# Optimization experiments

Measured on AMD Instinct MI355X. Metric: run time of the kernel, lower is better.

## Reference

```python
import jax, jax.numpy as jnp
import numpy as np

N = 50000   # nodes
E = 800000  # edges (before self loops)
IN_DIM = 64
HID = 128
HEADS = 4
DH = HID // HEADS  # 32 per-head out_feats
L = 3
EPS = 1e-5
NEG_SLOPE = 0.2


def setup_inputs() -> dict:
    key = jax.random.key(0)
    ks = jax.random.split(key, 10)
    s = 0.1  # weight scale for numerical sanity
    return {
        "node_feats": jax.random.normal(ks[0], (N, IN_DIM), jnp.float32),
        "src": jax.random.randint(ks[1], (E,), 0, N, dtype=jnp.int32),
        "dst": jax.random.randint(ks[2], (E,), 0, N, dtype=jnp.int32),
        "W_in": jax.random.normal(ks[3], (IN_DIM, HID), jnp.float32) * s,
        "b_in": jnp.zeros((HID,), jnp.float32),
        "W_src": jax.random.normal(ks[4], (L, HID, HID), jnp.float32) * s,
        "b_src": jnp.zeros((L, HID), jnp.float32),
        "W_dst": jax.random.normal(ks[5], (L, HID, HID), jnp.float32) * s,
        "b_dst": jnp.zeros((L, HID), jnp.float32),
        "attn": jax.random.normal(ks[6], (L, HEADS, DH), jnp.float32) * s,
        "ln_g": jnp.ones((L, HID), jnp.float32),
        "ln_b": jnp.zeros((L, HID), jnp.float32),
    }


def _layer_norm(x, g, b):
    mu = jnp.mean(x, axis=-1, keepdims=True)
    var = jnp.mean((x - mu) ** 2, axis=-1, keepdims=True)
    return (x - mu) * jax.lax.rsqrt(var + EPS) * g + b


def _gatv2(h, s_idx, d_idx, Ws, bs, Wd, bd, a):
    # h: [N, HID]; edges s_idx -> d_idx (self loops included)
    fs = (h @ Ws + bs).reshape(N, HEADS, DH)  # W_src h, source features
    fd = (h @ Wd + bd).reshape(N, HEADS, DH)  # W_dst h, dest features
    e = jax.nn.leaky_relu(fs[s_idx] + fd[d_idx], NEG_SLOPE)   # [E', H, D]
    logits = jnp.einsum('ehd,hd->eh', e, a)                   # [E', H]
    # segment softmax over incoming edges of each destination node
    m = jax.ops.segment_max(logits, d_idx, num_segments=N)    # [N, H]
    p = jnp.exp(logits - m[d_idx])
    z = jax.ops.segment_sum(p, d_idx, num_segments=N)         # [N, H]
    alpha = p / z[d_idx]                                      # [E', H]
    msg = fs[s_idx] * alpha[..., None]                        # [E', H, D]
    out = jax.ops.segment_sum(msg, d_idx, num_segments=N)     # [N, H, D]
    out = out + h.reshape(N, HEADS, DH)  # residual (Identity res_fc)
    return out.reshape(N, HID)


def reference(node_feats, src, dst, W_in, b_in, W_src, b_src, W_dst, b_dst, attn, ln_g, ln_b):
    loop = jnp.arange(N, dtype=src.dtype)
    s_idx = jnp.concatenate([src, loop])  # add_self_loop
    d_idx = jnp.concatenate([dst, loop])
    h = node_feats @ W_in + b_in
    for l in range(L):
        h_new = _gatv2(h, s_idx, d_idx, W_src[l], b_src[l], W_dst[l], b_dst[l], attn[l])
        h = _layer_norm(h + h_new, ln_g[l], ln_b[l])
        h = jax.nn.relu(h)
    graph_emb = jnp.mean(h, axis=0, keepdims=True)  # dgl.mean_nodes, batch of 1 graph
    return graph_emb, h
```

## Files before the change

kernel.cpp:

```cpp
#include <hip/hip_runtime.h>
#include <hip/hip_bf16.h>

#define NN 50000
#define CSTRIDE 16

typedef short short8 __attribute__((ext_vector_type(8)));
typedef float f32x4 __attribute__((ext_vector_type(4)));

#define GLOBAL_AS __attribute__((address_space(1)))
#define LDS_AS __attribute__((address_space(3)))

__device__ __forceinline__ unsigned short f2bf(float f) {
    unsigned int b = __float_as_uint(f);
    unsigned int r = (b + 0x7FFFu + ((b >> 16) & 1u)) >> 16;
    return (unsigned short)r;
}
__device__ __forceinline__ float bf2f(unsigned short u) {
    return __uint_as_float((unsigned int)u << 16);
}


__global__ void hist_rank_kernel(const int* __restrict__ dst, int* countsS,
                                 int* __restrict__ rank, int E) {
    int i = blockIdx.x * blockDim.x + threadIdx.x;
    if (i < E) rank[i] = atomicAdd(&countsS[(size_t)dst[i] * CSTRIDE], 1);
}

__global__ __launch_bounds__(256) void alloc_kernel(const int* __restrict__ countsS,
                                                    int* __restrict__ row_beg,
                                                    int* total, int n) {
    int i = blockIdx.x * blockDim.x + threadIdx.x;
    int lane = threadIdx.x & 63;
    int len = (i < n) ? (countsS[(size_t)i * CSTRIDE] + 1) : 0;
    int p = len;
    #pragma unroll
    for (int off = 1; off < 64; off <<= 1) {
        int t = __shfl_up(p, off);
        if (lane >= off) p += t;
    }
    int tot = __shfl(p, 63);
    int base = 0;
    if (lane == 63) base = atomicAdd(total, tot);
    base = __shfl(base, 63);
    if (i < n) row_beg[i] = base + p - len;
}

__global__ void scatter_kernel(const int* __restrict__ src, const int* __restrict__ dst,
                               const int* __restrict__ rank, const int* __restrict__ row_beg,
                               const int* __restrict__ countsS,
                               int* __restrict__ col, int E, int n) {
    int i = blockIdx.x * blockDim.x + threadIdx.x;
    if (i >= E + n) return;
    if (i < E) {
        col[row_beg[dst[i]] + rank[i]] = src[i];
    } else {
        int v = i - E;
        col[row_beg[v] + countsS[(size_t)v * CSTRIDE]] = v;
    }
}

__global__ __launch_bounds__(256) void convert_w_kernel(const float* __restrict__ Ws,
                                                        const float* __restrict__ Wd,
                                                        const float* __restrict__ Win,
                                                        unsigned short* __restrict__ WtL,
                                                        unsigned short* __restrict__ WtIn) {
    int blk = blockIdx.x;
    if (blk < 384) {
        int e = blk * 256 + threadIdx.x;
        int l = e >> 15;
        int r = e & 32767;
        int colc = r >> 7;
        int k = r & 127;
        float v = (colc < 128) ? Ws[l * 16384 + k * 128 + colc]
                               : Wd[l * 16384 + k * 128 + (colc - 128)];
        WtL[l * 32768 + colc * 128 + k] = f2bf(v);
    } else {
        int e = (blk - 384) * 256 + threadIdx.x;
        int colc = e >> 6;
        int k = e & 63;
        WtIn[colc * 64 + k] = f2bf(Win[k * 128 + colc]);
    }
}

__global__ __launch_bounds__(256, 4) void in_proj_mfma(const float* __restrict__ x,
                                                       const unsigned short* __restrict__ Wt,
                                                       const float* __restrict__ b,
                                                       unsigned short* __restrict__ hB) {
    int tid = threadIdx.x;
    int w = tid >> 6, l = tid & 63;
    int m = l & 15, q = l >> 4;
    short8 B[2][2];
    #pragma unroll
    for (int ct = 0; ct < 2; ++ct) {
        int col = w * 32 + ct * 16 + m;
        const unsigned short* wp = Wt + col * 64 + q * 8;
        #pragma unroll
        for (int kt = 0; kt < 2; ++kt) B[ct][kt] = *(const short8*)(wp + kt * 32);
    }
    float bias[2];
    #pragma unroll
    for (int ct = 0; ct < 2; ++ct) bias[ct] = b[w * 32 + ct * 16 + m];
    for (int rg = blockIdx.x; rg < NN / 16; rg += gridDim.x) {
        int row0 = rg * 16;
        const float* ap = x + (size_t)(row0 + m) * 64 + q * 8;
        short8 A[2];
        #pragma unroll
        for (int kt = 0; kt < 2; ++kt) {
            float4 f0 = *(const float4*)(ap + kt * 32);
            float4 f1 = *(const float4*)(ap + kt * 32 + 4);
            short8 a;
            a[0] = (short)f2bf(f0.x); a[1] = (short)f2bf(f0.y);
            a[2] = (short)f2bf(f0.z); a[3] = (short)f2bf(f0.w);
            a[4] = (short)f2bf(f1.x); a[5] = (short)f2bf(f1.y);
            a[6] = (short)f2bf(f1.z); a[7] = (short)f2bf(f1.w);
            A[kt] = a;
        }
        f32x4 acc[2];
        #pragma unroll
        for (int ct = 0; ct < 2; ++ct) acc[ct] = (f32x4){0.f, 0.f, 0.f, 0.f};
        #pragma unroll
        for (int kt = 0; kt < 2; ++kt)
            #pragma unroll
            for (int ct = 0; ct < 2; ++ct)
                acc[ct] = __builtin_amdgcn_mfma_f32_16x16x32_bf16(A[kt], B[ct][kt], acc[ct], 0, 0, 0);
        #pragma unroll
        for (int ct = 0; ct < 2; ++ct) {
            int col = w * 32 + ct * 16 + m;
            #pragma unroll
            for (int i = 0; i < 4; ++i) {
                int row = row0 + q * 4 + i;
                hB[(size_t)row * 128 + col] = f2bf(acc[ct][i] + bias[ct]);
            }
        }
    }
}

__global__ __launch_bounds__(256, 4) void dual_gemm_mfma(const unsigned short* __restrict__ hB,
                                                         const unsigned short* __restrict__ Wt,
                                                         const float* __restrict__ bs,
                                                         const float* __restrict__ bd,
                                                         unsigned short* __restrict__ fsB,
                                                         unsigned short* __restrict__ fdB) {
    __shared__ unsigned short Atile[64 * 128];
    int tid = threadIdx.x;
    int w = tid >> 6, l = tid & 63;
    int m = l & 15, q = l >> 4;
    short8 B[4][4];
    #pragma unroll
    for (int ct = 0; ct < 4; ++ct) {
        int col = w * 64 + ct * 16 + m;
        const unsigned short* wp = Wt + col * 128 + q * 8;
        #pragma unroll
        for (int kt = 0; kt < 4; ++kt) B[ct][kt] = *(const short8*)(wp + kt * 32);
    }
    const float* bptr = (w < 2) ? bs : bd;
    unsigned short* OUT = (w < 2) ? fsB : fdB;
    int ocb = (w * 64) & 127;
    float bias[4];
    #pragma unroll
    for (int ct = 0; ct < 4; ++ct) bias[ct] = bptr[ocb + ct * 16 + m];

    const int NT = (NN + 63) / 64;
    for (int t = blockIdx.x; t < NT; t += gridDim.x) {
        int row0 = t * 64;
        const char* gsrc = (const char*)(hB + (size_t)row0 * 128);
        #pragma unroll
        for (int c = 0; c < 4; ++c) {
            int off = c * 4096 + tid * 16;
            __builtin_amdgcn_global_load_lds((const GLOBAL_AS void*)(gsrc + off),
                                             (LDS_AS void*)((char*)Atile + off), 16, 0, 0);
        }
        __syncthreads();
        #pragma unroll
        for (int rg = 0; rg < 4; ++rg) {
            const unsigned short* ap = Atile + (rg * 16 + m) * 128 + q * 8;
            short8 A[4];
            #pragma unroll
            for (int kt = 0; kt < 4; ++kt) A[kt] = *(const short8*)(ap + kt * 32);
            f32x4 acc[4];
            #pragma unroll
            for (int ct = 0; ct < 4; ++ct) acc[ct] = (f32x4){0.f, 0.f, 0.f, 0.f};
            #pragma unroll
            for (int kt = 0; kt < 4; ++kt)
                #pragma unroll
                for (int ct = 0; ct < 4; ++ct)
                    acc[ct] = __builtin_amdgcn_mfma_f32_16x16x32_bf16(A[kt], B[ct][kt], acc[ct], 0, 0, 0);
            #pragma unroll
            for (int ct = 0; ct < 4; ++ct) {
                int col = ocb + ct * 16 + m;
                #pragma unroll
                for (int i = 0; i < 4; ++i) {
                    int row = row0 + rg * 16 + q * 4 + i;
                    if (row < NN) OUT[(size_t)row * 128 + col] = f2bf(acc[ct][i] + bias[ct]);
                }
            }
        }
        __syncthreads();
    }
}

__global__ __launch_bounds__(256) void agg_ln_kernel(const unsigned short* __restrict__ h_in,
                                                     const unsigned short* __restrict__ fsB,
                                                     const unsigned short* __restrict__ fdB,
                                                     const int* __restrict__ row_beg,
                                                     const int* __restrict__ countsS,
                                                     const int* __restrict__ col,
                                                     const float* __restrict__ attn,
                                                     const float* __restrict__ ln_g,
                                                     const float* __restrict__ ln_b,
                                                     unsigned short* __restrict__ hb_out,
                                                     float* __restrict__ hf_out, int n) {
    int gwave = (blockIdx.x * blockDim.x + threadIdx.x) >> 6;
    int lane = threadIdx.x & 63;
    int half = lane >> 5;
    int sub = lane & 31;
    int node = gwave * 2 + half;
    if (node >= n) return;
    int f0 = 4 * sub;
    ushort4 ud = *(const ushort4*)(fdB + (size_t)node * 128 + f0);
    float4 fd4;
    fd4.x = bf2f(ud.x); fd4.y = bf2f(ud.y); fd4.z = bf2f(ud.z); fd4.w = bf2f(ud.w);
    ushort4 uh = *(const ushort4*)(h_in + (size_t)node * 128 + f0);
    float4 h4;
    h4.x = bf2f(uh.x); h4.y = bf2f(uh.y); h4.z = bf2f(uh.z); h4.w = bf2f(uh.w);
    const float4 a4 = *(const float4*)(attn + f0);
    int beg = row_beg[node], end = beg + countsS[(size_t)node * CSTRIDE] + 1;

    float z[4];
    float4 acc[4];
    #pragma unroll
    for (int k = 0; k < 4; ++k) {
        z[k] = 0.f;
        acc[k].x = 0.f; acc[k].y = 0.f; acc[k].z = 0.f; acc[k].w = 0.f;
    }

    int j = beg;
    for (; j + 3 < end; j += 4) {
        int s0 = col[j], s1 = col[j + 1], s2 = col[j + 2], s3 = col[j + 3];
        ushort4 u0 = *(const ushort4*)(fsB + (size_t)s0 * 128 + f0);
        ushort4 u1 = *(const ushort4*)(fsB + (size_t)s1 * 128 + f0);
        ushort4 u2 = *(const ushort4*)(fsB + (size_t)s2 * 128 + f0);
        ushort4 u3 = *(const ushort4*)(fsB + (size_t)s3 * 128 + f0);
        float4 v0, v1, v2, v3;
        v0.x = bf2f(u0.x); v0.y = bf2f(u0.y); v0.z = bf2f(u0.z); v0.w = bf2f(u0.w);
        v1.x = bf2f(u1.x); v1.y = bf2f(u1.y); v1.z = bf2f(u1.z); v1.w = bf2f(u1.w);
        v2.x = bf2f(u2.x); v2.y = bf2f(u2.y); v2.z = bf2f(u2.z); v2.w = bf2f(u2.w);
        v3.x = bf2f(u3.x); v3.y = bf2f(u3.y); v3.z = bf2f(u3.z); v3.w = bf2f(u3.w);
        float p0, p1, p2, p3;
        {
            float e0 = v0.x + fd4.x; e0 = fmaxf(e0, 0.2f * e0);
            float e1 = v0.y + fd4.y; e1 = fmaxf(e1, 0.2f * e1);
            float e2 = v0.z + fd4.z; e2 = fmaxf(e2, 0.2f * e2);
            float e3 = v0.w + fd4.w; e3 = fmaxf(e3, 0.2f * e3);
            p0 = e0 * a4.x + e1 * a4.y + e2 * a4.z + e3 * a4.w;
        }
        {
            float e0 = v1.x + fd4.x; e0 = fmaxf(e0, 0.2f * e0);
            float e1 = v1.y + fd4.y; e1 = fmaxf(e1, 0.2f * e1);
            float e2 = v1.z + fd4.z; e2 = fmaxf(e2, 0.2f * e2);
            float e3 = v1.w + fd4.w; e3 = fmaxf(e3, 0.2f * e3);
            p1 = e0 * a4.x + e1 * a4.y + e2 * a4.z + e3 * a4.w;
        }
        {
            float e0 = v2.x + fd4.x; e0 = fmaxf(e0, 0.2f * e0);
            float e1 = v2.y + fd4.y; e1 = fmaxf(e1, 0.2f * e1);
            float e2 = v2.z + fd4.z; e2 = fmaxf(e2, 0.2f * e2);
            float e3 = v2.w + fd4.w; e3 = fmaxf(e3, 0.2f * e3);
            p2 = e0 * a4.x + e1 * a4.y + e2 * a4.z + e3 * a4.w;
        }
        {
            float e0 = v3.x + fd4.x; e0 = fmaxf(e0, 0.2f * e0);
            float e1 = v3.y + fd4.y; e1 = fmaxf(e1, 0.2f * e1);
            float e2 = v3.z + fd4.z; e2 = fmaxf(e2, 0.2f * e2);
            float e3 = v3.w + fd4.w; e3 = fmaxf(e3, 0.2f * e3);
            p3 = e0 * a4.x + e1 * a4.y + e2 * a4.z + e3 * a4.w;
        }
        #pragma unroll
        for (int off = 1; off <= 4; off <<= 1) {
            p0 += __shfl_xor(p0, off);
            p1 += __shfl_xor(p1, off);
            p2 += __shfl_xor(p2, off);
            p3 += __shfl_xor(p3, off);
        }
        float w0 = __expf(p0), w1 = __expf(p1), w2 = __expf(p2), w3 = __expf(p3);
        z[0] += w0; z[1] += w1; z[2] += w2; z[3] += w3;
        acc[0].x += w0 * v0.x; acc[0].y += w0 * v0.y; acc[0].z += w0 * v0.z; acc[0].w += w0 * v0.w;
        acc[1].x += w1 * v1.x; acc[1].y += w1 * v1.y; acc[1].z += w1 * v1.z; acc[1].w += w1 * v1.w;
        acc[2].x += w2 * v2.x; acc[2].y += w2 * v2.y; acc[2].z += w2 * v2.z; acc[2].w += w2 * v2.w;
        acc[3].x += w3 * v3.x; acc[3].y += w3 * v3.y; acc[3].z += w3 * v3.z; acc[3].w += w3 * v3.w;
    }
    for (; j < end; ++j) {
        int s = col[j];
        ushort4 u = *(const ushort4*)(fsB + (size_t)s * 128 + f0);
        float4 v;
        v.x = bf2f(u.x); v.y = bf2f(u.y); v.z = bf2f(u.z); v.w = bf2f(u.w);
        float e0 = v.x + fd4.x; e0 = fmaxf(e0, 0.2f * e0);
        float e1 = v.y + fd4.y; e1 = fmaxf(e1, 0.2f * e1);
        float e2 = v.z + fd4.z; e2 = fmaxf(e2, 0.2f * e2);
        float e3 = v.w + fd4.w; e3 = fmaxf(e3, 0.2f * e3);
        float p = e0 * a4.x + e1 * a4.y + e2 * a4.z + e3 * a4.w;
        p += __shfl_xor(p, 1);
        p += __shfl_xor(p, 2);
        p += __shfl_xor(p, 4);
        float w = __expf(p);
        z[0] += w;
        acc[0].x += w * v.x; acc[0].y += w * v.y; acc[0].z += w * v.z; acc[0].w += w * v.w;
    }
    float zT = (z[0] + z[1]) + (z[2] + z[3]);
    float axT = (acc[0].x + acc[1].x) + (acc[2].x + acc[3].x);
    float ayT = (acc[0].y + acc[1].y) + (acc[2].y + acc[3].y);
    float azT = (acc[0].z + acc[1].z) + (acc[2].z + acc[3].z);
    float awT = (acc[0].w + acc[1].w) + (acc[2].w + acc[3].w);
    float inv = 1.0f / zT;
    float x0 = 2.f * h4.x + axT * inv;
    float x1 = 2.f * h4.y + ayT * inv;
    float x2 = 2.f * h4.z + azT * inv;
    float x3 = 2.f * h4.w + awT * inv;
    float s = (x0 + x1) + (x2 + x3);
    #pragma unroll
    for (int off = 1; off <= 16; off <<= 1) s += __shfl_xor(s, off);
    float mean = s * (1.f / 128.f);
    float d0 = x0 - mean, d1 = x1 - mean, d2 = x2 - mean, d3 = x3 - mean;
    float v = (d0 * d0 + d1 * d1) + (d2 * d2 + d3 * d3);
    #pragma unroll
    for (int off = 1; off <= 16; off <<= 1) v += __shfl_xor(v, off);
    float rstd = rsqrtf(v * (1.f / 128.f) + 1e-5f);
    float4 g4 = *(const float4*)(ln_g + f0);
    float4 bb4 = *(const float4*)(ln_b + f0);
    float4 o;
    o.x = fmaxf(d0 * rstd * g4.x + bb4.x, 0.f);
    o.y = fmaxf(d1 * rstd * g4.y + bb4.y, 0.f);
    o.z = fmaxf(d2 * rstd * g4.z + bb4.z, 0.f);
    o.w = fmaxf(d3 * rstd * g4.w + bb4.w, 0.f);
    if (hf_out) {
        *(float4*)(hf_out + (size_t)node * 128 + f0) = o;
    } else {
        ushort4 ob;
        ob.x = f2bf(o.x); ob.y = f2bf(o.y); ob.z = f2bf(o.z); ob.w = f2bf(o.w);
        *(ushort4*)(hb_out + (size_t)node * 128 + f0) = ob;
    }
}


__global__ __launch_bounds__(128) void mean1_kernel(const float* __restrict__ h,
                                                    float* __restrict__ partials, int n) {
    int c = threadIdx.x;
    float acc = 0.f;
    for (int r = blockIdx.x; r < n; r += gridDim.x)
        acc += h[(size_t)r * 128 + c];
    partials[blockIdx.x * 128 + c] = acc;
}

__global__ __launch_bounds__(1024) void mean2_kernel(const float* __restrict__ partials,
                                                     float* __restrict__ out, int nb, int n) {
    __shared__ float smem[8][128];
    int c = threadIdx.x & 127;
    int g = threadIdx.x >> 7;
    float acc = 0.f;
    for (int r = g; r < nb; r += 8)
        acc += partials[r * 128 + c];
    smem[g][c] = acc;
    __syncthreads();
    if (threadIdx.x < 128) {
        float s = 0.f;
        #pragma unroll
        for (int k = 0; k < 8; ++k) s += smem[k][c];
        out[c] = s * (1.f / n);
    }
}

extern "C" void kernel_launch(void* const* d_in, const int* in_sizes, int n_in,
                              void* d_out, int out_size, void* d_ws, size_t ws_size,
                              hipStream_t stream) {
    const float* node_feats = (const float*)d_in[0];
    const int* src = (const int*)d_in[1];
    const int* dst = (const int*)d_in[2];
    const float* W_in = (const float*)d_in[3];
    const float* b_in = (const float*)d_in[4];
    const float* W_src = (const float*)d_in[5];
    const float* b_src = (const float*)d_in[6];
    const float* W_dst = (const float*)d_in[7];
    const float* b_dst = (const float*)d_in[8];
    const float* attn = (const float*)d_in[9];
    const float* ln_g = (const float*)d_in[10];
    const float* ln_b = (const float*)d_in[11];
    float* out = (float*)d_out;

    const int N = NN;
    const int E = in_sizes[1];

    unsigned short* fsB = (unsigned short*)d_ws;
    unsigned short* fdB = fsB + (size_t)N * 128;
    unsigned short* hB = fdB + (size_t)N * 128;
    unsigned short* WtL = hB + (size_t)N * 128;
    unsigned short* WtIn = WtL + 3 * 32768;
    int* countsS = (int*)(WtIn + 8192);
    int* total = countsS + (size_t)N * CSTRIDE;
    int* row_beg = total + 1;
    int* rankb = row_beg + N;
    int* colb = rankb + E;
    float* partials = (float*)(colb + (E + N));

    hipMemsetAsync(countsS, 0, ((size_t)N * CSTRIDE + 1) * sizeof(int), stream);
    hist_rank_kernel<<<(E + 255) / 256, 256, 0, stream>>>(dst, countsS, rankb, E);
    alloc_kernel<<<(N + 255) / 256, 256, 0, stream>>>(countsS, row_beg, total, N);
    scatter_kernel<<<(E + N + 255) / 256, 256, 0, stream>>>(src, dst, rankb, row_beg,
                                                            countsS, colb, E, N);

    convert_w_kernel<<<416, 256, 0, stream>>>(W_src, W_dst, W_in, WtL, WtIn);

    in_proj_mfma<<<512, 256, 0, stream>>>(node_feats, WtIn, b_in, hB);

    const int NT = (N + 63) / 64;
    for (int l = 0; l < 3; ++l) {
        int last = (l == 2);
        dual_gemm_mfma<<<NT, 256, 0, stream>>>(hB, WtL + (size_t)l * 32768,
                                               b_src + l * 128, b_dst + l * 128,
                                               fsB, fdB);
        agg_ln_kernel<<<(N + 7) / 8, 256, 0, stream>>>(hB, fsB, fdB, row_beg, countsS, colb,
                                                       attn + l * 128, ln_g + l * 128,
                                                       ln_b + l * 128,
                                                       last ? nullptr : hB,
                                                       last ? (out + 128) : nullptr, N);
    }

    mean1_kernel<<<256, 128, 0, stream>>>(out + 128, partials, N);
    mean2_kernel<<<1, 1024, 0, stream>>>(partials, out, 256, N);
}
```

Before: 423.4 us.

## Fuse setup kernels and make aggregation persistent with cheaper LeakyReLU math

Merges the histogram, weight conversion and input projection into one prep kernel, and merges the CSR scatter with the layer-0 dual GEMM into one launch. The input projection now reads W_in directly instead of a transposed copy. The aggregation kernel becomes a grid-stride loop over nodes with a fixed 2048 blocks, uses 32-bit shifted addressing, and rewrites LeakyReLU as a linear term plus an abs term. The goal is fewer launches and less per-edge ALU work, at the cost of heterogeneous blocks inside a launch and a possible occupancy change.

```diff
diff --git a/kernel.cpp b/kernel.cpp
--- a/kernel.cpp
+++ b/kernel.cpp
@@ -20,10 +20,83 @@
 }
 
 
-__global__ void hist_rank_kernel(const int* __restrict__ dst, int* countsS,
-                                 int* __restrict__ rank, int E) {
-    int i = blockIdx.x * blockDim.x + threadIdx.x;
-    if (i < E) rank[i] = atomicAdd(&countsS[(size_t)dst[i] * CSTRIDE], 1);
+__global__ __launch_bounds__(256, 4) void prep_kernel(
+        const int* __restrict__ dst, int* countsS, int* __restrict__ rank, int E,
+        const float* __restrict__ Ws, const float* __restrict__ Wd,
+        unsigned short* __restrict__ WtL,
+        const float* __restrict__ x, const float* __restrict__ Win,
+        const float* __restrict__ bin, unsigned short* __restrict__ hB) {
+    int HB = (E + 255) >> 8;
+    int blk = blockIdx.x;
+    if (blk < HB) {
+        int i = blk * 256 + threadIdx.x;
+        if (i < E) rank[i] = atomicAdd(&countsS[(size_t)dst[i] * CSTRIDE], 1);
+        return;
+    }
+    if (blk < HB + 384) {
+        int e = (blk - HB) * 256 + threadIdx.x;
+        int l = e >> 15;
+        int r = e & 32767;
+        int colc = r >> 7;
+        int k = r & 127;
+        float v = (colc < 128) ? Ws[l * 16384 + k * 128 + colc]
+                               : Wd[l * 16384 + k * 128 + (colc - 128)];
+        WtL[l * 32768 + colc * 128 + k] = f2bf(v);
+        return;
+    }
+    int blk0 = blk - HB - 384;
+    int tid = threadIdx.x;
+    int w = tid >> 6, l = tid & 63;
+    int m = l & 15, q = l >> 4;
+    short8 B[2][2];
+    #pragma unroll
+    for (int ct = 0; ct < 2; ++ct) {
+        int colw = w * 32 + ct * 16 + m;
+        #pragma unroll
+        for (int kt = 0; kt < 2; ++kt) {
+            short8 a;
+            #pragma unroll
+            for (int jj = 0; jj < 8; ++jj)
+                a[jj] = (short)f2bf(Win[(kt * 32 + q * 8 + jj) * 128 + colw]);
+            B[ct][kt] = a;
+        }
+    }
+    float bias[2];
+    #pragma unroll
+    for (int ct = 0; ct < 2; ++ct) bias[ct] = bin[w * 32 + ct * 16 + m];
+    for (int rg = blk0; rg < NN / 16; rg += 512) {
+        int row0 = rg * 16;
+        const float* ap = x + (size_t)(row0 + m) * 64 + q * 8;
+        short8 A[2];
+        #pragma unroll
+        for (int kt = 0; kt < 2; ++kt) {
+            float4 f0 = *(const float4*)(ap + kt * 32);
+            float4 f1 = *(const float4*)(ap + kt * 32 + 4);
+            short8 a;
+            a[0] = (short)f2bf(f0.x); a[1] = (short)f2bf(f0.y);
+            a[2] = (short)f2bf(f0.z); a[3] = (short)f2bf(f0.w);
+            a[4] = (short)f2bf(f1.x); a[5] = (short)f2bf(f1.y);
+            a[6] = (short)f2bf(f1.z); a[7] = (short)f2bf(f1.w);
+            A[kt] = a;
+        }
+        f32x4 acc[2];
+        #pragma unroll
+        for (int ct = 0; ct < 2; ++ct) acc[ct] = (f32x4){0.f, 0.f, 0.f, 0.f};
+        #pragma unroll
+        for (int kt = 0; kt < 2; ++kt)
+            #pragma unroll
+            for (int ct = 0; ct < 2; ++ct)
+                acc[ct] = __builtin_amdgcn_mfma_f32_16x16x32_bf16(A[kt], B[ct][kt], acc[ct], 0, 0, 0);
+        #pragma unroll
+        for (int ct = 0; ct < 2; ++ct) {
+            int colw = w * 32 + ct * 16 + m;
+            #pragma unroll
+            for (int i = 0; i < 4; ++i) {
+                int row = row0 + q * 4 + i;
+                hB[(size_t)row * 128 + colw] = f2bf(acc[ct][i] + bias[ct]);
+            }
+        }
+    }
 }
 
 __global__ __launch_bounds__(256) void alloc_kernel(const int* __restrict__ countsS,
@@ -45,94 +118,91 @@
     if (i < n) row_beg[i] = base + p - len;
 }
 
-__global__ void scatter_kernel(const int* __restrict__ src, const int* __restrict__ dst,
-                               const int* __restrict__ rank, const int* __restrict__ row_beg,
-                               const int* __restrict__ countsS,
-                               int* __restrict__ col, int E, int n) {
-    int i = blockIdx.x * blockDim.x + threadIdx.x;
-    if (i >= E + n) return;
-    if (i < E) {
-        col[row_beg[dst[i]] + rank[i]] = src[i];
-    } else {
-        int v = i - E;
-        col[row_beg[v] + countsS[(size_t)v * CSTRIDE]] = v;
-    }
-}
-
-__global__ __launch_bounds__(256) void convert_w_kernel(const float* __restrict__ Ws,
-                                                        const float* __restrict__ Wd,
-                                                        const float* __restrict__ Win,
-                                                        unsigned short* __restrict__ WtL,
-                                                        unsigned short* __restrict__ WtIn) {
-    int blk = blockIdx.x;
-    if (blk < 384) {
-        int e = blk * 256 + threadIdx.x;
-        int l = e >> 15;
-        int r = e & 32767;
-        int colc = r >> 7;
-        int k = r & 127;
-        float v = (colc < 128) ? Ws[l * 16384 + k * 128 + colc]
-                               : Wd[l * 16384 + k * 128 + (colc - 128)];
-        WtL[l * 32768 + colc * 128 + k] = f2bf(v);
-    } else {
-        int e = (blk - 384) * 256 + threadIdx.x;
-        int colc = e >> 6;
-        int k = e & 63;
-        WtIn[colc * 64 + k] = f2bf(Win[k * 128 + colc]);
-    }
-}
-
-__global__ __launch_bounds__(256, 4) void in_proj_mfma(const float* __restrict__ x,
-                                                       const unsigned short* __restrict__ Wt,
-                                                       const float* __restrict__ b,
-                                                       unsigned short* __restrict__ hB) {
+__device__ __forceinline__ void dual_body(const unsigned short* __restrict__ hB,
+                                          const unsigned short* __restrict__ Wt,
+                                          const float* __restrict__ bs,
+                                          const float* __restrict__ bd,
+                                          unsigned short* __restrict__ fsB,
+                                          unsigned short* __restrict__ fdB,
+                                          unsigned short* Atile, int t0, int tstride) {
     int tid = threadIdx.x;
     int w = tid >> 6, l = tid & 63;
     int m = l & 15, q = l >> 4;
-    short8 B[2][2];
+    short8 B[4][4];
     #pragma unroll
-    for (int ct = 0; ct < 2; ++ct) {
-        int col = w * 32 + ct * 16 + m;
-        const unsigned short* wp = Wt + col * 64 + q * 8;
-        #pragma unroll
-        for (int kt = 0; kt < 2; ++kt) B[ct][kt] = *(const short8*)(wp + kt * 32);
-    }
-    float bias[2];
+    for (int ct = 0; ct < 4; ++ct) {
+        int colw = w * 64 + ct * 16 + m;
+        const unsigned short* wp = Wt + colw * 128 + q * 8;
+        #pragma unroll
+        for (int kt = 0; kt < 4; ++kt) B[ct][kt] = *(const short8*)(wp + kt * 32);
+    }
+    const float* bptr = (w < 2) ? bs : bd;
+    unsigned short* OUT = (w < 2) ? fsB : fdB;
+    int ocb = (w * 64) & 127;
+    float bias[4];
     #pragma unroll
-    for (int ct = 0; ct < 2; ++ct) bias[ct] = b[w * 32 + ct * 16 + m];
-    for (int rg = blockIdx.x; rg < NN / 16; rg += gridDim.x) {
-        int row0 = rg * 16;
-        const float* ap = x + (size_t)(row0 + m) * 64 + q * 8;
-        short8 A[2];
-        #pragma unroll
-        for (int kt = 0; kt < 2; ++kt) {
-            float4 f0 = *(const float4*)(ap + kt * 32);
-            float4 f1 = *(const float4*)(ap + kt * 32 + 4);
-            short8 a;
-            a[0] = (short)f2bf(f0.x); a[1] = (short)f2bf(f0.y);
-            a[2] = (short)f2bf(f0.z); a[3] = (short)f2bf(f0.w);
-            a[4] = (short)f2bf(f1.x); a[5] = (short)f2bf(f1.y);
-            a[6] = (short)f2bf(f1.z); a[7] = (short)f2bf(f1.w);
-            A[kt] = a;
-        }
-        f32x4 acc[2];
-        #pragma unroll
-        for (int ct = 0; ct < 2; ++ct) acc[ct] = (f32x4){0.f, 0.f, 0.f, 0.f};
-        #pragma unroll
-        for (int kt = 0; kt < 2; ++kt)
-            #pragma unroll
-            for (int ct = 0; ct < 2; ++ct)
-                acc[ct] = __builtin_amdgcn_mfma_f32_16x16x32_bf16(A[kt], B[ct][kt], acc[ct], 0, 0, 0);
-        #pragma unroll
-        for (int ct = 0; ct < 2; ++ct) {
-            int col = w * 32 + ct * 16 + m;
-            #pragma unroll
-            for (int i = 0; i < 4; ++i) {
-                int row = row0 + q * 4 + i;
-                hB[(size_t)row * 128 + col] = f2bf(acc[ct][i] + bias[ct]);
-            }
-        }
-    }
+    for (int ct = 0; ct < 4; ++ct) bias[ct] = bptr[ocb + ct * 16 + m];
+
+    const int NT = (NN + 63) / 64;
+    for (int t = t0; t < NT; t += tstride) {
+        int row0 = t * 64;
+        const char* gsrc = (const char*)(hB + (size_t)row0 * 128);
+        #pragma unroll
+        for (int c = 0; c < 4; ++c) {
+            int off = c * 4096 + tid * 16;
+            __builtin_amdgcn_global_load_lds((const GLOBAL_AS void*)(gsrc + off),
+                                             (LDS_AS void*)((char*)Atile + off), 16, 0, 0);
+        }
+        __syncthreads();
+        #pragma unroll
+        for (int rg = 0; rg < 4; ++rg) {
+            const unsigned short* ap = Atile + (rg * 16 + m) * 128 + q * 8;
+            short8 A[4];
+            #pragma unroll
+            for (int kt = 0; kt < 4; ++kt) A[kt] = *(const short8*)(ap + kt * 32);
+            f32x4 acc[4];
+            #pragma unroll
+            for (int ct = 0; ct < 4; ++ct) acc[ct] = (f32x4){0.f, 0.f, 0.f, 0.f};
+            #pragma unroll
+            for (int kt = 0; kt < 4; ++kt)
+                #pragma unroll
+                for (int ct = 0; ct < 4; ++ct)
+                    acc[ct] = __builtin_amdgcn_mfma_f32_16x16x32_bf16(A[kt], B[ct][kt], acc[ct], 0, 0, 0);
+            #pragma unroll
+            for (int ct = 0; ct < 4; ++ct) {
+                int colw = ocb + ct * 16 + m;
+                #pragma unroll
+                for (int i = 0; i < 4; ++i) {
+                    int row = row0 + rg * 16 + q * 4 + i;
+                    if (row < NN) OUT[(size_t)row * 128 + colw] = f2bf(acc[ct][i] + bias[ct]);
+                }
+            }
+        }
+        __syncthreads();
+    }
+}
+
+__global__ __launch_bounds__(256, 4) void scatter_dual_kernel(
+        const int* __restrict__ src, const int* __restrict__ dst,
+        const int* __restrict__ rank, const int* __restrict__ row_beg,
+        const int* __restrict__ countsS, int* __restrict__ col, int E, int n,
+        const unsigned short* __restrict__ hB, const unsigned short* __restrict__ Wt,
+        const float* __restrict__ bs, const float* __restrict__ bd,
+        unsigned short* __restrict__ fsB, unsigned short* __restrict__ fdB) {
+    __shared__ unsigned short Atile[64 * 128];
+    int SB = (E + n + 255) >> 8;
+    if ((int)blockIdx.x < SB) {
+        int i = blockIdx.x * 256 + threadIdx.x;
+        if (i >= E + n) return;
+        if (i < E) {
+            col[row_beg[dst[i]] + rank[i]] = src[i];
+        } else {
+            int v = i - E;
+            col[row_beg[v] + countsS[(size_t)v * CSTRIDE]] = v;
+        }
+        return;
+    }
+    dual_body(hB, Wt, bs, bd, fsB, fdB, Atile, blockIdx.x - SB, gridDim.x - SB);
 }
 
 __global__ __launch_bounds__(256, 4) void dual_gemm_mfma(const unsigned short* __restrict__ hB,
@@ -142,61 +212,7 @@
                                                          unsigned short* __restrict__ fsB,
                                                          unsigned short* __restrict__ fdB) {
     __shared__ unsigned short Atile[64 * 128];
-    int tid = threadIdx.x;
-    int w = tid >> 6, l = tid & 63;
-    int m = l & 15, q = l >> 4;
-    short8 B[4][4];
-    #pragma unroll
-    for (int ct = 0; ct < 4; ++ct) {
-        int col = w * 64 + ct * 16 + m;
-        const unsigned short* wp = Wt + col * 128 + q * 8;
-        #pragma unroll
-        for (int kt = 0; kt < 4; ++kt) B[ct][kt] = *(const short8*)(wp + kt * 32);
-    }
-    const float* bptr = (w < 2) ? bs : bd;
-    unsigned short* OUT = (w < 2) ? fsB : fdB;
-    int ocb = (w * 64) & 127;
-    float bias[4];
-    #pragma unroll
-    for (int ct = 0; ct < 4; ++ct) bias[ct] = bptr[ocb + ct * 16 + m];
-
-    const int NT = (NN + 63) / 64;
-    for (int t = blockIdx.x; t < NT; t += gridDim.x) {
-        int row0 = t * 64;
-        const char* gsrc = (const char*)(hB + (size_t)row0 * 128);
-        #pragma unroll
-        for (int c = 0; c < 4; ++c) {
-            int off = c * 4096 + tid * 16;
-            __builtin_amdgcn_global_load_lds((const GLOBAL_AS void*)(gsrc + off),
-                                             (LDS_AS void*)((char*)Atile + off), 16, 0, 0);
-        }
-        __syncthreads();
-        #pragma unroll
-        for (int rg = 0; rg < 4; ++rg) {
-            const unsigned short* ap = Atile + (rg * 16 + m) * 128 + q * 8;
-            short8 A[4];
-            #pragma unroll
-            for (int kt = 0; kt < 4; ++kt) A[kt] = *(const short8*)(ap + kt * 32);
-            f32x4 acc[4];
-            #pragma unroll
-            for (int ct = 0; ct < 4; ++ct) acc[ct] = (f32x4){0.f, 0.f, 0.f, 0.f};
-            #pragma unroll
-            for (int kt = 0; kt < 4; ++kt)
-                #pragma unroll
-                for (int ct = 0; ct < 4; ++ct)
-                    acc[ct] = __builtin_amdgcn_mfma_f32_16x16x32_bf16(A[kt], B[ct][kt], acc[ct], 0, 0, 0);
-            #pragma unroll
-            for (int ct = 0; ct < 4; ++ct) {
-                int col = ocb + ct * 16 + m;
-                #pragma unroll
-                for (int i = 0; i < 4; ++i) {
-                    int row = row0 + rg * 16 + q * 4 + i;
-                    if (row < NN) OUT[(size_t)row * 128 + col] = f2bf(acc[ct][i] + bias[ct]);
-                }
-            }
-        }
-        __syncthreads();
-    }
+    dual_body(hB, Wt, bs, bd, fsB, fdB, Atile, blockIdx.x, gridDim.x);
 }
 
 __global__ __launch_bounds__(256) void agg_ln_kernel(const unsigned short* __restrict__ h_in,
@@ -210,134 +226,134 @@
                                                      const float* __restrict__ ln_b,
                                                      unsigned short* __restrict__ hb_out,
                                                      float* __restrict__ hf_out, int n) {
-    int gwave = (blockIdx.x * blockDim.x + threadIdx.x) >> 6;
     int lane = threadIdx.x & 63;
     int half = lane >> 5;
     int sub = lane & 31;
-    int node = gwave * 2 + half;
-    if (node >= n) return;
     int f0 = 4 * sub;
-    ushort4 ud = *(const ushort4*)(fdB + (size_t)node * 128 + f0);
-    float4 fd4;
-    fd4.x = bf2f(ud.x); fd4.y = bf2f(ud.y); fd4.z = bf2f(ud.z); fd4.w = bf2f(ud.w);
-    ushort4 uh = *(const ushort4*)(h_in + (size_t)node * 128 + f0);
-    float4 h4;
-    h4.x = bf2f(uh.x); h4.y = bf2f(uh.y); h4.z = bf2f(uh.z); h4.w = bf2f(uh.w);
+    unsigned foff = (unsigned)(f0 * 2);
     const float4 a4 = *(const float4*)(attn + f0);
-    int beg = row_beg[node], end = beg + countsS[(size_t)node * CSTRIDE] + 1;
-
-    float z[4];
-    float4 acc[4];
-    #pragma unroll
-    for (int k = 0; k < 4; ++k) {
-        z[k] = 0.f;
-        acc[k].x = 0.f; acc[k].y = 0.f; acc[k].z = 0.f; acc[k].w = 0.f;
-    }
-
-    int j = beg;
-    for (; j + 3 < end; j += 4) {
-        int s0 = col[j], s1 = col[j + 1], s2 = col[j + 2], s3 = col[j + 3];
-        ushort4 u0 = *(const ushort4*)(fsB + (size_t)s0 * 128 + f0);
-        ushort4 u1 = *(const ushort4*)(fsB + (size_t)s1 * 128 + f0);
-        ushort4 u2 = *(const ushort4*)(fsB + (size_t)s2 * 128 + f0);
-        ushort4 u3 = *(const ushort4*)(fsB + (size_t)s3 * 128 + f0);
-        float4 v0, v1, v2, v3;
-        v0.x = bf2f(u0.x); v0.y = bf2f(u0.y); v0.z = bf2f(u0.z); v0.w = bf2f(u0.w);
-        v1.x = bf2f(u1.x); v1.y = bf2f(u1.y); v1.z = bf2f(u1.z); v1.w = bf2f(u1.w);
-        v2.x = bf2f(u2.x); v2.y = bf2f(u2.y); v2.z = bf2f(u2.z); v2.w = bf2f(u2.w);
-        v3.x = bf2f(u3.x); v3.y = bf2f(u3.y); v3.z = bf2f(u3.z); v3.w = bf2f(u3.w);
-        float p0, p1, p2, p3;
-        {
-            float e0 = v0.x + fd4.x; e0 = fmaxf(e0, 0.2f * e0);
-            float e1 = v0.y + fd4.y; e1 = fmaxf(e1, 0.2f * e1);
-            float e2 = v0.z + fd4.z; e2 = fmaxf(e2, 0.2f * e2);
-            float e3 = v0.w + fd4.w; e3 = fmaxf(e3, 0.2f * e3);
-            p0 = e0 * a4.x + e1 * a4.y + e2 * a4.z + e3 * a4.w;
-        }
-        {
-            float e0 = v1.x + fd4.x; e0 = fmaxf(e0, 0.2f * e0);
-            float e1 = v1.y + fd4.y; e1 = fmaxf(e1, 0.2f * e1);
-            float e2 = v1.z + fd4.z; e2 = fmaxf(e2, 0.2f * e2);
-            float e3 = v1.w + fd4.w; e3 = fmaxf(e3, 0.2f * e3);
-            p1 = e0 * a4.x + e1 * a4.y + e2 * a4.z + e3 * a4.w;
-        }
-        {
-            float e0 = v2.x + fd4.x; e0 = fmaxf(e0, 0.2f * e0);
-            float e1 = v2.y + fd4.y; e1 = fmaxf(e1, 0.2f * e1);
-            float e2 = v2.z + fd4.z; e2 = fmaxf(e2, 0.2f * e2);
-            float e3 = v2.w + fd4.w; e3 = fmaxf(e3, 0.2f * e3);
-            p2 = e0 * a4.x + e1 * a4.y + e2 * a4.z + e3 * a4.w;
-        }
-        {
-            float e0 = v3.x + fd4.x; e0 = fmaxf(e0, 0.2f * e0);
-            float e1 = v3.y + fd4.y; e1 = fmaxf(e1, 0.2f * e1);
-            float e2 = v3.z + fd4.z; e2 = fmaxf(e2, 0.2f * e2);
-            float e3 = v3.w + fd4.w; e3 = fmaxf(e3, 0.2f * e3);
-            p3 = e0 * a4.x + e1 * a4.y + e2 * a4.z + e3 * a4.w;
-        }
-        #pragma unroll
-        for (int off = 1; off <= 4; off <<= 1) {
-            p0 += __shfl_xor(p0, off);
-            p1 += __shfl_xor(p1, off);
-            p2 += __shfl_xor(p2, off);
-            p3 += __shfl_xor(p3, off);
-        }
-        float w0 = __expf(p0), w1 = __expf(p1), w2 = __expf(p2), w3 = __expf(p3);
-        z[0] += w0; z[1] += w1; z[2] += w2; z[3] += w3;
-        acc[0].x += w0 * v0.x; acc[0].y += w0 * v0.y; acc[0].z += w0 * v0.z; acc[0].w += w0 * v0.w;
-        acc[1].x += w1 * v1.x; acc[1].y += w1 * v1.y; acc[1].z += w1 * v1.z; acc[1].w += w1 * v1.w;
-        acc[2].x += w2 * v2.x; acc[2].y += w2 * v2.y; acc[2].z += w2 * v2.z; acc[2].w += w2 * v2.w;
-        acc[3].x += w3 * v3.x; acc[3].y += w3 * v3.y; acc[3].z += w3 * v3.z; acc[3].w += w3 * v3.w;
-    }
-    for (; j < end; ++j) {
-        int s = col[j];
-        ushort4 u = *(const ushort4*)(fsB + (size_t)s * 128 + f0);
-        float4 v;
-        v.x = bf2f(u.x); v.y = bf2f(u.y); v.z = bf2f(u.z); v.w = bf2f(u.w);
-        float e0 = v.x + fd4.x; e0 = fmaxf(e0, 0.2f * e0);
-        float e1 = v.y + fd4.y; e1 = fmaxf(e1, 0.2f * e1);
-        float e2 = v.z + fd4.z; e2 = fmaxf(e2, 0.2f * e2);
-        float e3 = v.w + fd4.w; e3 = fmaxf(e3, 0.2f * e3);
-        float p = e0 * a4.x + e1 * a4.y + e2 * a4.z + e3 * a4.w;
-        p += __shfl_xor(p, 1);
-        p += __shfl_xor(p, 2);
-        p += __shfl_xor(p, 4);
-        float w = __expf(p);
-        z[0] += w;
-        acc[0].x += w * v.x; acc[0].y += w * v.y; acc[0].z += w * v.z; acc[0].w += w * v.w;
-    }
-    float zT = (z[0] + z[1]) + (z[2] + z[3]);
-    float axT = (acc[0].x + acc[1].x) + (acc[2].x + acc[3].x);
-    float ayT = (acc[0].y + acc[1].y) + (acc[2].y + acc[3].y);
-    float azT = (acc[0].z + acc[1].z) + (acc[2].z + acc[3].z);
-    float awT = (acc[0].w + acc[1].w) + (acc[2].w + acc[3].w);
-    float inv = 1.0f / zT;
-    float x0 = 2.f * h4.x + axT * inv;
-    float x1 = 2.f * h4.y + ayT * inv;
-    float x2 = 2.f * h4.z + azT * inv;
-    float x3 = 2.f * h4.w + awT * inv;
-    float s = (x0 + x1) + (x2 + x3);
-    #pragma unroll
-    for (int off = 1; off <= 16; off <<= 1) s += __shfl_xor(s, off);
-    float mean = s * (1.f / 128.f);
-    float d0 = x0 - mean, d1 = x1 - mean, d2 = x2 - mean, d3 = x3 - mean;
-    float v = (d0 * d0 + d1 * d1) + (d2 * d2 + d3 * d3);
-    #pragma unroll
-    for (int off = 1; off <= 16; off <<= 1) v += __shfl_xor(v, off);
-    float rstd = rsqrtf(v * (1.f / 128.f) + 1e-5f);
-    float4 g4 = *(const float4*)(ln_g + f0);
-    float4 bb4 = *(const float4*)(ln_b + f0);
-    float4 o;
-    o.x = fmaxf(d0 * rstd * g4.x + bb4.x, 0.f);
-    o.y = fmaxf(d1 * rstd * g4.y + bb4.y, 0.f);
-    o.z = fmaxf(d2 * rstd * g4.z + bb4.z, 0.f);
-    o.w = fmaxf(d3 * rstd * g4.w + bb4.w, 0.f);
-    if (hf_out) {
-        *(float4*)(hf_out + (size_t)node * 128 + f0) = o;
-    } else {
-        ushort4 ob;
-        ob.x = f2bf(o.x); ob.y = f2bf(o.y); ob.z = f2bf(o.z); ob.w = f2bf(o.w);
-        *(ushort4*)(hb_out + (size_t)node * 128 + f0) = ob;
+    float4 a06, a04;
+    a06.x = 0.6f * a4.x; a06.y = 0.6f * a4.y; a06.z = 0.6f * a4.z; a06.w = 0.6f * a4.w;
+    a04.x = 0.4f * a4.x; a04.y = 0.4f * a4.y; a04.z = 0.4f * a4.z; a04.w = 0.4f * a4.w;
+    const float4 g4 = *(const float4*)(ln_g + f0);
+    const float4 bb4 = *(const float4*)(ln_b + f0);
+    const char* fsp = (const char*)fsB;
+
+    int gwave = (int)((blockIdx.x * blockDim.x + threadIdx.x) >> 6);
+    int nw = (int)((gridDim.x * blockDim.x) >> 6);
+    int npairs = (n + 1) >> 1;
+    for (int pr = gwave; pr < npairs; pr += nw) {
+        int node = pr * 2 + half;
+        if (node >= n) continue;
+        ushort4 ud = *(const ushort4*)((const char*)fdB + (((unsigned)node << 8) | foff));
+        float4 fd4;
+        fd4.x = bf2f(ud.x); fd4.y = bf2f(ud.y); fd4.z = bf2f(ud.z); fd4.w = bf2f(ud.w);
+        ushort4 uh = *(const ushort4*)((const char*)h_in + (((unsigned)node << 8) | foff));
+        float4 h4;
+        h4.x = bf2f(uh.x); h4.y = bf2f(uh.y); h4.z = bf2f(uh.z); h4.w = bf2f(uh.w);
+        int beg = row_beg[node], end = beg + countsS[(size_t)node * CSTRIDE] + 1;
+
+        float z[4];
+        float4 acc[4];
+        #pragma unroll
+        for (int k = 0; k < 4; ++k) {
+            z[k] = 0.f;
+            acc[k].x = 0.f; acc[k].y = 0.f; acc[k].z = 0.f; acc[k].w = 0.f;
+        }
+
+        int j = beg;
+        for (; j + 3 < end; j += 4) {
+            int s0 = col[j], s1 = col[j + 1], s2 = col[j + 2], s3 = col[j + 3];
+            ushort4 u0 = *(const ushort4*)(fsp + (((unsigned)s0 << 8) | foff));
+            ushort4 u1 = *(const ushort4*)(fsp + (((unsigned)s1 << 8) | foff));
+            ushort4 u2 = *(const ushort4*)(fsp + (((unsigned)s2 << 8) | foff));
+            ushort4 u3 = *(const ushort4*)(fsp + (((unsigned)s3 << 8) | foff));
+            float4 v0, v1, v2, v3;
+            v0.x = bf2f(u0.x); v0.y = bf2f(u0.y); v0.z = bf2f(u0.z); v0.w = bf2f(u0.w);
+            v1.x = bf2f(u1.x); v1.y = bf2f(u1.y); v1.z = bf2f(u1.z); v1.w = bf2f(u1.w);
+            v2.x = bf2f(u2.x); v2.y = bf2f(u2.y); v2.z = bf2f(u2.z); v2.w = bf2f(u2.w);
+            v3.x = bf2f(u3.x); v3.y = bf2f(u3.y); v3.z = bf2f(u3.z); v3.w = bf2f(u3.w);
+            float p0, p1, p2, p3;
+            {
+                float e0 = v0.x + fd4.x, e1 = v0.y + fd4.y, e2 = v0.z + fd4.z, e3 = v0.w + fd4.w;
+                p0 = e0 * a06.x + fabsf(e0) * a04.x + e1 * a06.y + fabsf(e1) * a04.y
+                   + e2 * a06.z + fabsf(e2) * a04.z + e3 * a06.w + fabsf(e3) * a04.w;
+            }
+            {
+                float e0 = v1.x + fd4.x, e1 = v1.y + fd4.y, e2 = v1.z + fd4.z, e3 = v1.w + fd4.w;
+                p1 = e0 * a06.x + fabsf(e0) * a04.x + e1 * a06.y + fabsf(e1) * a04.y
+                   + e2 * a06.z + fabsf(e2) * a04.z + e3 * a06.w + fabsf(e3) * a04.w;
+            }
+            {
+                float e0 = v2.x + fd4.x, e1 = v2.y + fd4.y, e2 = v2.z + fd4.z, e3 = v2.w + fd4.w;
+                p2 = e0 * a06.x + fabsf(e0) * a04.x + e1 * a06.y + fabsf(e1) * a04.y
+                   + e2 * a06.z + fabsf(e2) * a04.z + e3 * a06.w + fabsf(e3) * a04.w;
+            }
+            {
+                float e0 = v3.x + fd4.x, e1 = v3.y + fd4.y, e2 = v3.z + fd4.z, e3 = v3.w + fd4.w;
+                p3 = e0 * a06.x + fabsf(e0) * a04.x + e1 * a06.y + fabsf(e1) * a04.y
+                   + e2 * a06.z + fabsf(e2) * a04.z + e3 * a06.w + fabsf(e3) * a04.w;
+            }
+            #pragma unroll
+            for (int off = 1; off <= 4; off <<= 1) {
+                p0 += __shfl_xor(p0, off);
+                p1 += __shfl_xor(p1, off);
+                p2 += __shfl_xor(p2, off);
+                p3 += __shfl_xor(p3, off);
+            }
+            float w0 = __expf(p0), w1 = __expf(p1), w2 = __expf(p2), w3 = __expf(p3);
+            z[0] += w0; z[1] += w1; z[2] += w2; z[3] += w3;
+            acc[0].x += w0 * v0.x; acc[0].y += w0 * v0.y; acc[0].z += w0 * v0.z; acc[0].w += w0 * v0.w;
+            acc[1].x += w1 * v1.x; acc[1].y += w1 * v1.y; acc[1].z += w1 * v1.z; acc[1].w += w1 * v1.w;
+            acc[2].x += w2 * v2.x; acc[2].y += w2 * v2.y; acc[2].z += w2 * v2.z; acc[2].w += w2 * v2.w;
+            acc[3].x += w3 * v3.x; acc[3].y += w3 * v3.y; acc[3].z += w3 * v3.z; acc[3].w += w3 * v3.w;
+        }
+        for (; j < end; ++j) {
+            int s = col[j];
+            ushort4 u = *(const ushort4*)(fsp + (((unsigned)s << 8) | foff));
+            float4 v;
+            v.x = bf2f(u.x); v.y = bf2f(u.y); v.z = bf2f(u.z); v.w = bf2f(u.w);
+            float e0 = v.x + fd4.x, e1 = v.y + fd4.y, e2 = v.z + fd4.z, e3 = v.w + fd4.w;
+            float p = e0 * a06.x + fabsf(e0) * a04.x + e1 * a06.y + fabsf(e1) * a04.y
+                    + e2 * a06.z + fabsf(e2) * a04.z + e3 * a06.w + fabsf(e3) * a04.w;
+            p += __shfl_xor(p, 1);
+            p += __shfl_xor(p, 2);
+            p += __shfl_xor(p, 4);
+            float w = __expf(p);
+            z[0] += w;
+            acc[0].x += w * v.x; acc[0].y += w * v.y; acc[0].z += w * v.z; acc[0].w += w * v.w;
+        }
+        float zT = (z[0] + z[1]) + (z[2] + z[3]);
+        float axT = (acc[0].x + acc[1].x) + (acc[2].x + acc[3].x);
+        float ayT = (acc[0].y + acc[1].y) + (acc[2].y + acc[3].y);
+        float azT = (acc[0].z + acc[1].z) + (acc[2].z + acc[3].z);
+        float awT = (acc[0].w + acc[1].w) + (acc[2].w + acc[3].w);
+        float inv = 1.0f / zT;
+        float x0 = 2.f * h4.x + axT * inv;
+        float x1 = 2.f * h4.y + ayT * inv;
+        float x2 = 2.f * h4.z + azT * inv;
+        float x3 = 2.f * h4.w + awT * inv;
+        float s = (x0 + x1) + (x2 + x3);
+        #pragma unroll
+        for (int off = 1; off <= 16; off <<= 1) s += __shfl_xor(s, off);
+        float mean = s * (1.f / 128.f);
+        float d0 = x0 - mean, d1 = x1 - mean, d2 = x2 - mean, d3 = x3 - mean;
+        float v = (d0 * d0 + d1 * d1) + (d2 * d2 + d3 * d3);
+        #pragma unroll
+        for (int off = 1; off <= 16; off <<= 1) v += __shfl_xor(v, off);
+        float rstd = rsqrtf(v * (1.f / 128.f) + 1e-5f);
+        float4 o;
+        o.x = fmaxf(d0 * rstd * g4.x + bb4.x, 0.f);
+        o.y = fmaxf(d1 * rstd * g4.y + bb4.y, 0.f);
+        o.z = fmaxf(d2 * rstd * g4.z + bb4.z, 0.f);
+        o.w = fmaxf(d3 * rstd * g4.w + bb4.w, 0.f);
+        if (hf_out) {
+            *(float4*)((char*)hf_out + (((unsigned)node << 9) | (unsigned)(f0 * 4))) = o;
+        } else {
+            ushort4 ob;
+            ob.x = f2bf(o.x); ob.y = f2bf(o.y); ob.z = f2bf(o.z); ob.w = f2bf(o.w);
+            *(ushort4*)((char*)hb_out + (((unsigned)node << 8) | foff)) = ob;
+        }
     }
 }
 
@@ -401,27 +417,31 @@
     int* colb = rankb + E;
     float* partials = (float*)(colb + (E + N));
 
+    const int NT = (N + 63) / 64;
+
     hipMemsetAsync(countsS, 0, ((size_t)N * CSTRIDE + 1) * sizeof(int), stream);
-    hist_rank_kernel<<<(E + 255) / 256, 256, 0, stream>>>(dst, countsS, rankb, E);
+    int HB = (E + 255) / 256;
+    prep_kernel<<<HB + 384 + 512, 256, 0, stream>>>(dst, countsS, rankb, E,
+                                                    W_src, W_dst, WtL,
+                                                    node_feats, W_in, b_in, hB);
     alloc_kernel<<<(N + 255) / 256, 256, 0, stream>>>(countsS, row_beg, total, N);
-    scatter_kernel<<<(E + N + 255) / 256, 256, 0, stream>>>(src, dst, rankb, row_beg,
-                                                            countsS, colb, E, N);
-
-    convert_w_kernel<<<416, 256, 0, stream>>>(W_src, W_dst, W_in, WtL, WtIn);
-
-    in_proj_mfma<<<512, 256, 0, stream>>>(node_feats, WtIn, b_in, hB);
-
-    const int NT = (N + 63) / 64;
+
+    int SB = (E + N + 255) / 256;
+    scatter_dual_kernel<<<SB + NT, 256, 0, stream>>>(src, dst, rankb, row_beg,
+                                                     countsS, colb, E, N,
+                                                     hB, WtL, b_src, b_dst, fsB, fdB);
+
     for (int l = 0; l < 3; ++l) {
         int last = (l == 2);
-        dual_gemm_mfma<<<NT, 256, 0, stream>>>(hB, WtL + (size_t)l * 32768,
-                                               b_src + l * 128, b_dst + l * 128,
-                                               fsB, fdB);
-        agg_ln_kernel<<<(N + 7) / 8, 256, 0, stream>>>(hB, fsB, fdB, row_beg, countsS, colb,
-                                                       attn + l * 128, ln_g + l * 128,
-                                                       ln_b + l * 128,
-                                                       last ? nullptr : hB,
-                                                       last ? (out + 128) : nullptr, N);
+        if (l > 0)
+            dual_gemm_mfma<<<NT, 256, 0, stream>>>(hB, WtL + (size_t)l * 32768,
+                                                   b_src + l * 128, b_dst + l * 128,
+                                                   fsB, fdB);
+        agg_ln_kernel<<<2048, 256, 0, stream>>>(hB, fsB, fdB, row_beg, countsS, colb,
+                                                attn + l * 128, ln_g + l * 128,
+                                                ln_b + l * 128,
+                                                last ? nullptr : hB,
+                                                last ? (out + 128) : nullptr, N);
     }
 
     mean1_kernel<<<256, 128, 0, stream>>>(out + 128, partials, N);
```

After: 446.0 us. +5.3%, slower.
